# Optimization experiments

Hardware: AMD Instinct MI355X
Metric: run time of the kernel (lower is better)

The kernel has to match this reference:

```python
import jax, jax.numpy as jnp
import numpy as np

D_MODEL, D_K, D_V = 1024, 64, 128
NUM_HEAD = D_MODEL // D_V  # 8


def setup_inputs() -> dict:
    key = jax.random.key(0)
    ks = jax.random.split(key, 6)
    B, SQ, SKV = 4, 2048, 2048
    return {
        "encoder_output": jax.random.normal(ks[0], (B, SKV, D_MODEL), jnp.float32),
        "pre_output": jax.random.normal(ks[1], (B, SQ, D_MODEL), jnp.float32),
        "Wq": jax.random.normal(ks[2], (D_MODEL, D_K * NUM_HEAD), jnp.float32) * 0.02,
        "Wk": jax.random.normal(ks[3], (D_MODEL, D_K * NUM_HEAD), jnp.float32) * 0.02,
        "Wv": jax.random.normal(ks[4], (D_MODEL, D_MODEL), jnp.float32) * 0.02,
        "Wo": jax.random.normal(ks[5], (D_MODEL, D_MODEL), jnp.float32) * 0.02,
    }


def reference(encoder_output, pre_output, Wq, Wk, Wv, Wo):
    B, SQ, _ = pre_output.shape
    SKV = encoder_output.shape[1]
    # projections (Linear, bias=False)
    q = pre_output @ Wq          # [B, SQ, H*d_k]
    k = encoder_output @ Wk      # [B, SKV, H*d_k]
    v = encoder_output @ Wv      # [B, SKV, H*d_v] (= d_model)
    # per-head contiguous slices == reshape into head dim
    q = q.reshape(B, SQ, NUM_HEAD, D_K)
    k = k.reshape(B, SKV, NUM_HEAD, D_K)
    v = v.reshape(B, SKV, NUM_HEAD, D_V)
    scale = 1.0 / np.sqrt(D_K).astype(np.float32)
    scores = jnp.einsum("bqhd,bkhd->bhqk", q, k) * scale  # [B,H,SQ,SKV]
    attn = jax.nn.softmax(scores, axis=-1)
    out = jnp.einsum("bhqk,bkhd->bqhd", attn, v)           # [B,SQ,H,d_v]
    out = out.reshape(B, SQ, NUM_HEAD * D_V)               # concat heads
    return out @ Wo
```

## Files before the change

kernel.cpp:

```cpp
#include <hip/hip_runtime.h>
#include <math.h>

#define D_MODEL 1024
#define DK 64
#define DV 128
#define NH 8
#define BB 4
#define SQL 2048
#define SKV 2048

typedef __bf16 bf16x8 __attribute__((ext_vector_type(8)));
typedef float f32x4 __attribute__((ext_vector_type(4)));

__device__ __forceinline__ ushort f2bf(float f) {
  unsigned u = __float_as_uint(f);
  u += 0x7FFFu + ((u >> 16) & 1u);
  return (ushort)(u >> 16);
}

#define GLDS16(g, l)                                                       \
  __builtin_amdgcn_global_load_lds(                                        \
      (const __attribute__((address_space(1))) unsigned int*)(g),          \
      (__attribute__((address_space(3))) unsigned int*)(l), 16, 0, 0)

__global__ __launch_bounds__(256) void cvt_bf16_kernel(
    const float* __restrict__ src, ushort* __restrict__ dst, int n4) {
  int i = blockIdx.x * 256 + threadIdx.x;
  if (i >= n4) return;
  float4 v = ((const float4*)src)[i];
  ushort4 o;
  o.x = f2bf(v.x); o.y = f2bf(v.y); o.z = f2bf(v.z); o.w = f2bf(v.w);
  ((ushort4*)dst)[i] = o;
}

__global__ __launch_bounds__(256) void cvt_t_kernel(
    const float* __restrict__ W, ushort* __restrict__ Wt, int R, int C) {
  __shared__ ushort T[32][34];
  const int r0 = blockIdx.x * 32, c0 = blockIdx.y * 32;
  const int tx = threadIdx.x, ty = threadIdx.y;
#pragma unroll
  for (int i = 0; i < 4; ++i) {
    const int rr = ty + i * 8;
    T[rr][tx] = f2bf(W[(size_t)(r0 + rr) * C + c0 + tx]);
  }
  __syncthreads();
#pragma unroll
  for (int i = 0; i < 4; ++i) {
    const int rr = ty + i * 8;
    Wt[(size_t)(c0 + rr) * R + r0 + tx] = T[tx][rr];
  }
}

__global__ __launch_bounds__(256) void vtrans_kernel(
    const ushort* __restrict__ vb, ushort* __restrict__ vt) {
  __shared__ ushort T[32][34];
  const int s0 = blockIdx.x * 32;
  const int d0 = blockIdx.y * 32;
  const int bh = blockIdx.z;
  const int b = bh >> 3, h = bh & 7;
  const int tx = threadIdx.x, ty = threadIdx.y;
#pragma unroll
  for (int i = 0; i < 4; ++i) {
    const int rr = ty + i * 8;
    T[rr][tx] = vb[(size_t)(b * SKV + s0 + rr) * (NH * DV) + h * DV + d0 + tx];
  }
  __syncthreads();
#pragma unroll
  for (int i = 0; i < 4; ++i) {
    const int rr = ty + i * 8;
    vt[(size_t)bh * DV * SKV + (size_t)(d0 + rr) * SKV + s0 + tx] = T[tx][rr];
  }
}

template <typename OUT>
__global__ __launch_bounds__(256) void gemm_glds_kernel(
    const ushort* __restrict__ A0, const ushort* __restrict__ B0,
    OUT* __restrict__ C0, float osc0, const ushort* __restrict__ A1,
    const ushort* __restrict__ B1, OUT* __restrict__ C1, float osc1,
    int M, int N, int K) {
  __shared__ ushort As[128][32];
  __shared__ ushort Bs[128][32];
  const ushort* A = blockIdx.z ? A1 : A0;
  const ushort* Bt = blockIdx.z ? B1 : B0;
  OUT* C = blockIdx.z ? C1 : C0;
  const float osc = blockIdx.z ? osc1 : osc0;

  const int t = threadIdx.x;
  const int m0 = blockIdx.y * 128, n0 = blockIdx.x * 128;
  const int w = t >> 6, lane = t & 63;
  const int wm = (w >> 1) * 64, wn = (w & 1) * 64;
  const int lr = lane & 15, quad = lane >> 4;

  const int r0 = t >> 2;
  const int lb = (t & 3) ^ ((r0 >> 1) & 3);
  const ushort* gA0 = A + (size_t)(m0 + r0) * K + lb * 8;
  const ushort* gA1 = A + (size_t)(m0 + r0 + 64) * K + lb * 8;
  const ushort* gB0 = Bt + (size_t)(n0 + r0) * K + lb * 8;
  const ushort* gB1 = Bt + (size_t)(n0 + r0 + 64) * K + lb * 8;
  ushort* dA0 = (ushort*)As + t * 8;
  ushort* dA1 = (ushort*)As + t * 8 + 2048;
  ushort* dB0 = (ushort*)Bs + t * 8;
  ushort* dB1 = (ushort*)Bs + t * 8 + 2048;

  const int sw = (quad ^ ((lr >> 1) & 3)) * 8;

  f32x4 acc[4][4];
#pragma unroll
  for (int i = 0; i < 4; ++i)
#pragma unroll
    for (int j = 0; j < 4; ++j) acc[i][j] = (f32x4){0.f, 0.f, 0.f, 0.f};

  for (int k0 = 0; k0 < K; k0 += 32) {
    __syncthreads();
    GLDS16(gA0 + k0, dA0);
    GLDS16(gA1 + k0, dA1);
    GLDS16(gB0 + k0, dB0);
    GLDS16(gB1 + k0, dB1);
    __syncthreads();
    bf16x8 fa[4], fb[4];
#pragma unroll
    for (int i = 0; i < 4; ++i) fa[i] = *(const bf16x8*)&As[wm + i * 16 + lr][sw];
#pragma unroll
    for (int j = 0; j < 4; ++j) fb[j] = *(const bf16x8*)&Bs[wn + j * 16 + lr][sw];
#pragma unroll
    for (int i = 0; i < 4; ++i)
#pragma unroll
      for (int j = 0; j < 4; ++j)
        acc[i][j] = __builtin_amdgcn_mfma_f32_16x16x32_bf16(fa[i], fb[j],
                                                            acc[i][j], 0, 0, 0);
  }

#pragma unroll
  for (int i = 0; i < 4; ++i)
#pragma unroll
    for (int j = 0; j < 4; ++j)
#pragma unroll
      for (int r = 0; r < 4; ++r) {
        const int row = m0 + wm + i * 16 + quad * 4 + r;
        const int col = n0 + wn + j * 16 + lr;
        const float val = acc[i][j][r] * osc;
        if constexpr (sizeof(OUT) == 4)
          ((float*)C)[(size_t)row * N + col] = val;
        else
          ((ushort*)C)[(size_t)row * N + col] = f2bf(val);
      }
}

__global__ __launch_bounds__(256) void attn_mfma_kernel(
    const ushort* __restrict__ Q, const ushort* __restrict__ Kb,
    const ushort* __restrict__ Vt, ushort* __restrict__ Oo) {
  __shared__ ushort Ks[64][64];
  __shared__ ushort Vs[128][64];
  __shared__ ushort Ps[4][32][68];

  const int t = threadIdx.x;
  const int qt = blockIdx.x, h = blockIdx.y, b = blockIdx.z;
  const int w = t >> 6, lane = t & 63;
  const int lr = lane & 15, quad = lane >> 4;
  const int q0 = qt * 128 + w * 32;

  bf16x8 aq[2][2];
#pragma unroll
  for (int mt = 0; mt < 2; ++mt)
#pragma unroll
    for (int kh = 0; kh < 2; ++kh)
      aq[mt][kh] = *(const bf16x8*)&Q[(size_t)(b * SQL + q0 + mt * 16 + lr) *
                                          (NH * DK) +
                                      h * DK + kh * 32 + quad * 8];

  f32x4 accO[2][8];
#pragma unroll
  for (int mt = 0; mt < 2; ++mt)
#pragma unroll
    for (int dn = 0; dn < 8; ++dn) accO[mt][dn] = (f32x4){0.f, 0.f, 0.f, 0.f};
  float lsum[2] = {0.f, 0.f};

  const ushort* kbase = Kb + (size_t)b * SKV * (NH * DK) + h * DK;
  const ushort* vbase = Vt + (size_t)(b * NH + h) * DV * SKV;

  const int srow = t >> 3;
  const int slb = (t & 7) ^ (srow & 7);
  const ushort* gK0 = kbase + (size_t)srow * (NH * DK) + slb * 8;
  const ushort* gK1 = kbase + (size_t)(srow + 32) * (NH * DK) + slb * 8;
  ushort* dK0 = (ushort*)Ks + t * 8;
  ushort* dK1 = (ushort*)Ks + t * 8 + 2048;
  const ushort* gV[4];
  ushort* dV[4];
#pragma unroll
  for (int it = 0; it < 4; ++it) {
    gV[it] = vbase + (size_t)(srow + 32 * it) * SKV + slb * 8;
    dV[it] = (ushort*)Vs + t * 8 + 2048 * it;
  }

  const int sw8 = lr & 7;

  for (int kv0 = 0; kv0 < SKV; kv0 += 64) {
    __syncthreads();
    GLDS16(gK0 + (size_t)kv0 * (NH * DK), dK0);
    GLDS16(gK1 + (size_t)kv0 * (NH * DK), dK1);
#pragma unroll
    for (int it = 0; it < 4; ++it) GLDS16(gV[it] + kv0, dV[it]);
    __syncthreads();

#pragma unroll
    for (int nt = 0; nt < 4; ++nt) {
      const bf16x8 fk0 = *(const bf16x8*)&Ks[nt * 16 + lr][(quad ^ sw8) * 8];
      const bf16x8 fk1 =
          *(const bf16x8*)&Ks[nt * 16 + lr][((4 + quad) ^ sw8) * 8];
#pragma unroll
      for (int mt = 0; mt < 2; ++mt) {
        f32x4 s = (f32x4){0.f, 0.f, 0.f, 0.f};
        s = __builtin_amdgcn_mfma_f32_16x16x32_bf16(fk0, aq[mt][0], s, 0, 0, 0);
        s = __builtin_amdgcn_mfma_f32_16x16x32_bf16(fk1, aq[mt][1], s, 0, 0, 0);
        const unsigned u0 = __float_as_uint(exp2f(s[0]));
        const unsigned u1 = __float_as_uint(exp2f(s[1]));
        const unsigned u2 = __float_as_uint(exp2f(s[2]));
        const unsigned u3 = __float_as_uint(exp2f(s[3]));
        lsum[mt] += __uint_as_float(u0 & 0xffff0000u) +
                    __uint_as_float(u1 & 0xffff0000u) +
                    __uint_as_float(u2 & 0xffff0000u) +
                    __uint_as_float(u3 & 0xffff0000u);
        uint2 dd;
        dd.x = __builtin_amdgcn_perm(u1, u0, 0x07060302u);
        dd.y = __builtin_amdgcn_perm(u3, u2, 0x07060302u);
        *(uint2*)&Ps[w][mt * 16 + lr][nt * 16 + quad * 4] = dd;
      }
    }

    bf16x8 ap[2][2];
#pragma unroll
    for (int mt = 0; mt < 2; ++mt)
#pragma unroll
      for (int kh = 0; kh < 2; ++kh) {
        union { bf16x8 v; uint2 u[2]; } fr;
        fr.u[0] = *(const uint2*)&Ps[w][mt * 16 + lr][kh * 32 + quad * 8];
        fr.u[1] = *(const uint2*)&Ps[w][mt * 16 + lr][kh * 32 + quad * 8 + 4];
        ap[mt][kh] = fr.v;
      }

#pragma unroll
    for (int dn = 0; dn < 8; ++dn) {
      const bf16x8 fv0 = *(const bf16x8*)&Vs[dn * 16 + lr][(quad ^ sw8) * 8];
      const bf16x8 fv1 =
          *(const bf16x8*)&Vs[dn * 16 + lr][((4 + quad) ^ sw8) * 8];
#pragma unroll
      for (int mt = 0; mt < 2; ++mt) {
        accO[mt][dn] = __builtin_amdgcn_mfma_f32_16x16x32_bf16(
            ap[mt][0], fv0, accO[mt][dn], 0, 0, 0);
        accO[mt][dn] = __builtin_amdgcn_mfma_f32_16x16x32_bf16(
            ap[mt][1], fv1, accO[mt][dn], 0, 0, 0);
      }
    }
  }

  float lred[2];
#pragma unroll
  for (int mt = 0; mt < 2; ++mt) {
    float l = lsum[mt];
    l += __shfl_xor(l, 16);
    l += __shfl_xor(l, 32);
    lred[mt] = l;
  }
  float inv[2][4];
#pragma unroll
  for (int mt = 0; mt < 2; ++mt)
#pragma unroll
    for (int r = 0; r < 4; ++r) {
      const int srcb = (quad * 20 + r) * 4;
      const float lv = __int_as_float(
          __builtin_amdgcn_ds_bpermute(srcb, __float_as_int(lred[mt])));
      inv[mt][r] = 1.f / lv;
    }

#pragma unroll
  for (int mt = 0; mt < 2; ++mt)
#pragma unroll
    for (int dn = 0; dn < 8; ++dn)
#pragma unroll
      for (int r = 0; r < 4; ++r) {
        const size_t row = (size_t)b * SQL + q0 + mt * 16 + quad * 4 + r;
        Oo[row * D_MODEL + h * DV + dn * 16 + lr] =
            f2bf(accO[mt][dn][r] * inv[mt][r]);
      }
}

extern "C" void kernel_launch(void* const* d_in, const int* in_sizes, int n_in,
                              void* d_out, int out_size, void* d_ws,
                              size_t ws_size, hipStream_t stream) {
  const float* enc = (const float*)d_in[0];
  const float* pre = (const float*)d_in[1];
  const float* Wq = (const float*)d_in[2];
  const float* Wk = (const float*)d_in[3];
  const float* Wv = (const float*)d_in[4];
  const float* Wo = (const float*)d_in[5];
  float* out = (float*)d_out;

  const int M = BB * SQL;

  ushort* encb = (ushort*)d_ws;
  ushort* preb = encb + (size_t)M * D_MODEL;
  ushort* WqT = preb + (size_t)M * D_MODEL;
  ushort* WkT = WqT + (size_t)(NH * DK) * D_MODEL;
  ushort* WvT = WkT + (size_t)(NH * DK) * D_MODEL;
  ushort* WoT = WvT + (size_t)D_MODEL * D_MODEL;
  ushort* qb = WoT + (size_t)D_MODEL * D_MODEL;
  ushort* kb = qb + (size_t)M * (NH * DK);
  ushort* vt = kb + (size_t)M * (NH * DK);
  ushort* vb = preb;
  ushort* ao = encb;

  const int n4 = M * D_MODEL / 4;
  dim3 blk(256);
  dim3 tblk(32, 8);

  cvt_bf16_kernel<<<dim3(n4 / 256), blk, 0, stream>>>(enc, encb, n4);
  cvt_bf16_kernel<<<dim3(n4 / 256), blk, 0, stream>>>(pre, preb, n4);
  cvt_t_kernel<<<dim3(32, 16), tblk, 0, stream>>>(Wq, WqT, D_MODEL, NH * DK);
  cvt_t_kernel<<<dim3(32, 16), tblk, 0, stream>>>(Wk, WkT, D_MODEL, NH * DK);
  cvt_t_kernel<<<dim3(32, 32), tblk, 0, stream>>>(Wv, WvT, D_MODEL, D_MODEL);
  cvt_t_kernel<<<dim3(32, 32), tblk, 0, stream>>>(Wo, WoT, D_MODEL, D_MODEL);

  gemm_glds_kernel<ushort><<<dim3(4, 64, 2), blk, 0, stream>>>(
      preb, WqT, qb, 0.18033688011112042f, encb, WkT, kb, 1.0f, M, NH * DK,
      D_MODEL);
  gemm_glds_kernel<ushort><<<dim3(8, 64, 1), blk, 0, stream>>>(
      encb, WvT, vb, 1.0f, encb, WvT, vb, 1.0f, M, D_MODEL, D_MODEL);

  vtrans_kernel<<<dim3(SKV / 32, DV / 32, BB * NH), tblk, 0, stream>>>(vb, vt);

  attn_mfma_kernel<<<dim3(SQL / 128, NH, BB), blk, 0, stream>>>(qb, kb, vt, ao);

  gemm_glds_kernel<float><<<dim3(8, 64, 1), blk, 0, stream>>>(
      ao, WoT, out, 1.0f, ao, WoT, out, 1.0f, M, D_MODEL, D_MODEL);
}
```

Before: 309.4 us.

## Merge launches, fuse QKV GEMM, compute softmax row sums via MFMA

Combines the two input conversions and the four weight transposes into single launches, and merges the Q, K and V projections into one GEMM over a contiguous transposed weight buffer (WqT, WkT, WvT adjacent). This moves V out of the preb buffer to avoid aliasing. In attention, the per-row softmax denominator now comes from an extra MFMA against a ones vector instead of scalar adds plus shuffles and bpermute, and exp2 uses the hardware builtin. The goal is fewer launches, fewer VALU ops in the attention inner loop and better GPU fill for the projections, at the cost of extra MFMA work and accumulator registers.

```diff
diff --git a/kernel.cpp b/kernel.cpp
--- a/kernel.cpp
+++ b/kernel.cpp
@@ -12,6 +12,12 @@
 typedef __bf16 bf16x8 __attribute__((ext_vector_type(8)));
 typedef float f32x4 __attribute__((ext_vector_type(4)));
 
+#if __has_builtin(__builtin_amdgcn_exp2f)
+#define EXP2(x) __builtin_amdgcn_exp2f(x)
+#else
+#define EXP2(x) exp2f(x)
+#endif
+
 __device__ __forceinline__ ushort f2bf(float f) {
   unsigned u = __float_as_uint(f);
   u += 0x7FFFu + ((u >> 16) & 1u);
@@ -23,8 +29,11 @@
       (const __attribute__((address_space(1))) unsigned int*)(g),          \
       (__attribute__((address_space(3))) unsigned int*)(l), 16, 0, 0)
 
-__global__ __launch_bounds__(256) void cvt_bf16_kernel(
-    const float* __restrict__ src, ushort* __restrict__ dst, int n4) {
+__global__ __launch_bounds__(256) void cvt2_kernel(
+    const float* __restrict__ s0, const float* __restrict__ s1,
+    ushort* __restrict__ d0, ushort* __restrict__ d1, int n4) {
+  const float* src = blockIdx.z ? s1 : s0;
+  ushort* dst = blockIdx.z ? d1 : d0;
   int i = blockIdx.x * 256 + threadIdx.x;
   if (i >= n4) return;
   float4 v = ((const float4*)src)[i];
@@ -33,10 +42,20 @@
   ((ushort4*)dst)[i] = o;
 }
 
-__global__ __launch_bounds__(256) void cvt_t_kernel(
-    const float* __restrict__ W, ushort* __restrict__ Wt, int R, int C) {
+__global__ __launch_bounds__(256) void cvt_t4_kernel(
+    const float* __restrict__ W0, const float* __restrict__ W1,
+    const float* __restrict__ W2, const float* __restrict__ W3,
+    ushort* __restrict__ T0, ushort* __restrict__ T1, ushort* __restrict__ T2,
+    ushort* __restrict__ T3) {
   __shared__ ushort T[32][34];
-  const int r0 = blockIdx.x * 32, c0 = blockIdx.y * 32;
+  const int z = blockIdx.z;
+  const int C = (z < 2) ? 512 : 1024;
+  const int c0 = blockIdx.y * 32;
+  if (c0 >= C) return;
+  const float* W = (z == 0) ? W0 : (z == 1) ? W1 : (z == 2) ? W2 : W3;
+  ushort* Wt = (z == 0) ? T0 : (z == 1) ? T1 : (z == 2) ? T2 : T3;
+  const int R = 1024;
+  const int r0 = blockIdx.x * 32;
   const int tx = threadIdx.x, ty = threadIdx.y;
 #pragma unroll
   for (int i = 0; i < 4; ++i) {
@@ -73,30 +92,22 @@
 }
 
 template <typename OUT>
-__global__ __launch_bounds__(256) void gemm_glds_kernel(
-    const ushort* __restrict__ A0, const ushort* __restrict__ B0,
-    OUT* __restrict__ C0, float osc0, const ushort* __restrict__ A1,
-    const ushort* __restrict__ B1, OUT* __restrict__ C1, float osc1,
-    int M, int N, int K) {
-  __shared__ ushort As[128][32];
-  __shared__ ushort Bs[128][32];
-  const ushort* A = blockIdx.z ? A1 : A0;
-  const ushort* Bt = blockIdx.z ? B1 : B0;
-  OUT* C = blockIdx.z ? C1 : C0;
-  const float osc = blockIdx.z ? osc1 : osc0;
-
+__device__ __forceinline__ void gemm_tile_core(ushort (*As)[32],
+                                               ushort (*Bs)[32],
+                                               const ushort* At,
+                                               const ushort* Bt, OUT* Ct,
+                                               int ldc, float osc, int K) {
   const int t = threadIdx.x;
-  const int m0 = blockIdx.y * 128, n0 = blockIdx.x * 128;
   const int w = t >> 6, lane = t & 63;
   const int wm = (w >> 1) * 64, wn = (w & 1) * 64;
   const int lr = lane & 15, quad = lane >> 4;
 
   const int r0 = t >> 2;
   const int lb = (t & 3) ^ ((r0 >> 1) & 3);
-  const ushort* gA0 = A + (size_t)(m0 + r0) * K + lb * 8;
-  const ushort* gA1 = A + (size_t)(m0 + r0 + 64) * K + lb * 8;
-  const ushort* gB0 = Bt + (size_t)(n0 + r0) * K + lb * 8;
-  const ushort* gB1 = Bt + (size_t)(n0 + r0 + 64) * K + lb * 8;
+  const ushort* gA0 = At + (size_t)r0 * K + lb * 8;
+  const ushort* gA1 = At + (size_t)(r0 + 64) * K + lb * 8;
+  const ushort* gB0 = Bt + (size_t)r0 * K + lb * 8;
+  const ushort* gB1 = Bt + (size_t)(r0 + 64) * K + lb * 8;
   ushort* dA0 = (ushort*)As + t * 8;
   ushort* dA1 = (ushort*)As + t * 8 + 2048;
   ushort* dB0 = (ushort*)Bs + t * 8;
@@ -136,14 +147,48 @@
     for (int j = 0; j < 4; ++j)
 #pragma unroll
       for (int r = 0; r < 4; ++r) {
-        const int row = m0 + wm + i * 16 + quad * 4 + r;
-        const int col = n0 + wn + j * 16 + lr;
+        const int row = wm + i * 16 + quad * 4 + r;
+        const int col = wn + j * 16 + lr;
         const float val = acc[i][j][r] * osc;
         if constexpr (sizeof(OUT) == 4)
-          ((float*)C)[(size_t)row * N + col] = val;
+          ((float*)Ct)[(size_t)row * ldc + col] = val;
         else
-          ((ushort*)C)[(size_t)row * N + col] = f2bf(val);
-      }
+          ((ushort*)Ct)[(size_t)row * ldc + col] = f2bf(val);
+      }
+}
+
+__global__ __launch_bounds__(256) void gemm_qkv_kernel(
+    const ushort* __restrict__ preb, const ushort* __restrict__ encb,
+    const ushort* __restrict__ WqkvT, ushort* __restrict__ qb,
+    ushort* __restrict__ kb, ushort* __restrict__ vb, float qsc) {
+  __shared__ ushort As[128][32];
+  __shared__ ushort Bs[128][32];
+  const int n0 = blockIdx.x * 128, m0 = blockIdx.y * 128;
+  const int K = D_MODEL;
+  const ushort* A;
+  ushort* C;
+  int ldc, ncol;
+  float osc = 1.f;
+  if (n0 < 512) {
+    A = preb; C = qb; ldc = 512; ncol = n0; osc = qsc;
+  } else if (n0 < 1024) {
+    A = encb; C = kb; ldc = 512; ncol = n0 - 512;
+  } else {
+    A = encb; C = vb; ldc = 1024; ncol = n0 - 1024;
+  }
+  gemm_tile_core<ushort>(As, Bs, A + (size_t)m0 * K, WqkvT + (size_t)n0 * K,
+                         C + (size_t)m0 * ldc + ncol, ldc, osc, K);
+}
+
+__global__ __launch_bounds__(256) void gemm_o_kernel(
+    const ushort* __restrict__ ao, const ushort* __restrict__ WoT,
+    float* __restrict__ out) {
+  __shared__ ushort As[128][32];
+  __shared__ ushort Bs[128][32];
+  const int n0 = blockIdx.x * 128, m0 = blockIdx.y * 128;
+  const int K = D_MODEL;
+  gemm_tile_core<float>(As, Bs, ao + (size_t)m0 * K, WoT + (size_t)n0 * K,
+                        out + (size_t)m0 * D_MODEL + n0, D_MODEL, 1.f, K);
 }
 
 __global__ __launch_bounds__(256) void attn_mfma_kernel(
@@ -159,6 +204,10 @@
   const int lr = lane & 15, quad = lane >> 4;
   const int q0 = qt * 128 + w * 32;
 
+  union { bf16x8 v; ushort u[8]; } one8;
+#pragma unroll
+  for (int i = 0; i < 8; ++i) one8.u[i] = 0x3F80;
+
   bf16x8 aq[2][2];
 #pragma unroll
   for (int mt = 0; mt < 2; ++mt)
@@ -168,12 +217,11 @@
                                           (NH * DK) +
                                       h * DK + kh * 32 + quad * 8];
 
-  f32x4 accO[2][8];
+  f32x4 accO[2][9];
 #pragma unroll
   for (int mt = 0; mt < 2; ++mt)
 #pragma unroll
-    for (int dn = 0; dn < 8; ++dn) accO[mt][dn] = (f32x4){0.f, 0.f, 0.f, 0.f};
-  float lsum[2] = {0.f, 0.f};
+    for (int dn = 0; dn < 9; ++dn) accO[mt][dn] = (f32x4){0.f, 0.f, 0.f, 0.f};
 
   const ushort* kbase = Kb + (size_t)b * SKV * (NH * DK) + h * DK;
   const ushort* vbase = Vt + (size_t)(b * NH + h) * DV * SKV;
@@ -212,14 +260,10 @@
         f32x4 s = (f32x4){0.f, 0.f, 0.f, 0.f};
         s = __builtin_amdgcn_mfma_f32_16x16x32_bf16(fk0, aq[mt][0], s, 0, 0, 0);
         s = __builtin_amdgcn_mfma_f32_16x16x32_bf16(fk1, aq[mt][1], s, 0, 0, 0);
-        const unsigned u0 = __float_as_uint(exp2f(s[0]));
-        const unsigned u1 = __float_as_uint(exp2f(s[1]));
-        const unsigned u2 = __float_as_uint(exp2f(s[2]));
-        const unsigned u3 = __float_as_uint(exp2f(s[3]));
-        lsum[mt] += __uint_as_float(u0 & 0xffff0000u) +
-                    __uint_as_float(u1 & 0xffff0000u) +
-                    __uint_as_float(u2 & 0xffff0000u) +
-                    __uint_as_float(u3 & 0xffff0000u);
+        const unsigned u0 = __float_as_uint(EXP2(s[0]));
+        const unsigned u1 = __float_as_uint(EXP2(s[1]));
+        const unsigned u2 = __float_as_uint(EXP2(s[2]));
+        const unsigned u3 = __float_as_uint(EXP2(s[3]));
         uint2 dd;
         dd.x = __builtin_amdgcn_perm(u1, u0, 0x07060302u);
         dd.y = __builtin_amdgcn_perm(u3, u2, 0x07060302u);
@@ -251,37 +295,29 @@
             ap[mt][1], fv1, accO[mt][dn], 0, 0, 0);
       }
     }
-  }
-
-  float lred[2];
+#pragma unroll
+    for (int mt = 0; mt < 2; ++mt) {
+      accO[mt][8] = __builtin_amdgcn_mfma_f32_16x16x32_bf16(
+          ap[mt][0], one8.v, accO[mt][8], 0, 0, 0);
+      accO[mt][8] = __builtin_amdgcn_mfma_f32_16x16x32_bf16(
+          ap[mt][1], one8.v, accO[mt][8], 0, 0, 0);
+    }
+  }
+
 #pragma unroll
   for (int mt = 0; mt < 2; ++mt) {
-    float l = lsum[mt];
-    l += __shfl_xor(l, 16);
-    l += __shfl_xor(l, 32);
-    lred[mt] = l;
-  }
-  float inv[2][4];
-#pragma unroll
-  for (int mt = 0; mt < 2; ++mt)
-#pragma unroll
-    for (int r = 0; r < 4; ++r) {
-      const int srcb = (quad * 20 + r) * 4;
-      const float lv = __int_as_float(
-          __builtin_amdgcn_ds_bpermute(srcb, __float_as_int(lred[mt])));
-      inv[mt][r] = 1.f / lv;
-    }
-
-#pragma unroll
-  for (int mt = 0; mt < 2; ++mt)
+    float inv[4];
+#pragma unroll
+    for (int r = 0; r < 4; ++r) inv[r] = 1.f / accO[mt][8][r];
 #pragma unroll
     for (int dn = 0; dn < 8; ++dn)
 #pragma unroll
       for (int r = 0; r < 4; ++r) {
         const size_t row = (size_t)b * SQL + q0 + mt * 16 + quad * 4 + r;
         Oo[row * D_MODEL + h * DV + dn * 16 + lr] =
-            f2bf(accO[mt][dn][r] * inv[mt][r]);
-      }
+            f2bf(accO[mt][dn][r] * inv[r]);
+      }
+  }
 }
 
 extern "C" void kernel_launch(void* const* d_in, const int* in_sizes, int n_in,
@@ -306,30 +342,24 @@
   ushort* qb = WoT + (size_t)D_MODEL * D_MODEL;
   ushort* kb = qb + (size_t)M * (NH * DK);
   ushort* vt = kb + (size_t)M * (NH * DK);
-  ushort* vb = preb;
+  ushort* vb = vt + (size_t)M * D_MODEL;
   ushort* ao = encb;
 
   const int n4 = M * D_MODEL / 4;
   dim3 blk(256);
   dim3 tblk(32, 8);
 
-  cvt_bf16_kernel<<<dim3(n4 / 256), blk, 0, stream>>>(enc, encb, n4);
-  cvt_bf16_kernel<<<dim3(n4 / 256), blk, 0, stream>>>(pre, preb, n4);
-  cvt_t_kernel<<<dim3(32, 16), tblk, 0, stream>>>(Wq, WqT, D_MODEL, NH * DK);
-  cvt_t_kernel<<<dim3(32, 16), tblk, 0, stream>>>(Wk, WkT, D_MODEL, NH * DK);
-  cvt_t_kernel<<<dim3(32, 32), tblk, 0, stream>>>(Wv, WvT, D_MODEL, D_MODEL);
-  cvt_t_kernel<<<dim3(32, 32), tblk, 0, stream>>>(Wo, WoT, D_MODEL, D_MODEL);
-
-  gemm_glds_kernel<ushort><<<dim3(4, 64, 2), blk, 0, stream>>>(
-      preb, WqT, qb, 0.18033688011112042f, encb, WkT, kb, 1.0f, M, NH * DK,
-      D_MODEL);
-  gemm_glds_kernel<ushort><<<dim3(8, 64, 1), blk, 0, stream>>>(
-      encb, WvT, vb, 1.0f, encb, WvT, vb, 1.0f, M, D_MODEL, D_MODEL);
+  cvt2_kernel<<<dim3(n4 / 256, 1, 2), blk, 0, stream>>>(enc, pre, encb, preb,
+                                                        n4);
+  cvt_t4_kernel<<<dim3(32, 32, 4), tblk, 0, stream>>>(Wq, Wk, Wv, Wo, WqT, WkT,
+                                                      WvT, WoT);
+
+  gemm_qkv_kernel<<<dim3(16, 64), blk, 0, stream>>>(
+      preb, encb, WqT, qb, kb, vb, 0.18033688011112042f);
 
   vtrans_kernel<<<dim3(SKV / 32, DV / 32, BB * NH), tblk, 0, stream>>>(vb, vt);
 
   attn_mfma_kernel<<<dim3(SQL / 128, NH, BB), blk, 0, stream>>>(qb, kb, vt, ao);
 
-  gemm_glds_kernel<float><<<dim3(8, 64, 1), blk, 0, stream>>>(
-      ao, WoT, out, 1.0f, ao, WoT, out, 1.0f, M, D_MODEL, D_MODEL);
-}
+  gemm_o_kernel<<<dim3(8, 64), blk, 0, stream>>>(ao, WoT, out);
+}
```

New measurement: 284.4 us. 1.09x faster.
